# Performance work log

Hardware: AMD Instinct MI355X
Metric: run time of the kernel (lower is better)

Reference implementation:

```python
import jax, jax.numpy as jnp
import numpy as np

B, N, DIM = 2, 4096, 512
HEADS, DIM_HEAD = 8, 64
INNER = HEADS * DIM_HEAD  # 512
SCALE = DIM_HEAD ** -0.5
LN_EPS = 1e-5


def setup_inputs() -> dict:
    key = jax.random.key(0)
    ks = jax.random.split(key, 4)
    x = jax.random.normal(ks[0], (B, N, DIM), dtype=jnp.float32)
    # weights stored as [in, out] for plain matmul
    w_qkv = jax.random.normal(ks[1], (DIM, 3 * INNER), dtype=jnp.float32) * (DIM ** -0.5)
    ln_gamma = jnp.ones((INNER,), dtype=jnp.float32)
    ln_beta = jnp.zeros((INNER,), dtype=jnp.float32)
    w_out = jax.random.normal(ks[2], (INNER, DIM), dtype=jnp.float32) * (INNER ** -0.5)
    b_out = jnp.zeros((DIM,), dtype=jnp.float32)
    return {"x": x, "w_qkv": w_qkv, "ln_gamma": ln_gamma, "ln_beta": ln_beta,
            "w_out": w_out, "b_out": b_out}


def _layernorm(x, gamma, beta):
    mu = jnp.mean(x, axis=-1, keepdims=True)
    var = jnp.mean(jnp.square(x - mu), axis=-1, keepdims=True)
    return (x - mu) * jax.lax.rsqrt(var + LN_EPS) * gamma + beta


def reference(x, w_qkv, ln_gamma, ln_beta, w_out, b_out):
    b, n, _ = x.shape
    qkv = x @ w_qkv                                   # [b, n, 3*inner]
    q, k, v = jnp.split(qkv, 3, axis=-1)
    def to_heads(t):
        return t.reshape(b, n, HEADS, DIM_HEAD).transpose(0, 2, 1, 3)  # [b,h,n,d]
    q, k, v = to_heads(q), to_heads(k), to_heads(v)
    dots = jnp.einsum('bhid,bhjd->bhij', q, k) * SCALE  # [b,h,n,n]
    attn = jax.nn.relu(dots)                            # non-softmax rectified attention
    out = jnp.einsum('bhij,bhjd->bhid', attn, v)        # [b,h,n,d]
    out = out.transpose(0, 2, 1, 3).reshape(b, n, INNER)
    out = _layernorm(out, ln_gamma, ln_beta)
    return out @ w_out + b_out                          # [b,n,dim]
```

## Files before the change

kernel.cpp:

```cpp
#include <hip/hip_runtime.h>
#include <stdint.h>
#include <stddef.h>

typedef __bf16 bf16;
typedef bf16 bf16x4 __attribute__((ext_vector_type(4)));
typedef bf16 bf16x8 __attribute__((ext_vector_type(8)));
typedef float f32x4 __attribute__((ext_vector_type(4)));

#define DEVI static __device__ __forceinline__


DEVI f32x4 mfma16(bf16x8 a, bf16x8 b, f32x4 c) {
  return __builtin_amdgcn_mfma_f32_16x16x32_bf16(a, b, c, 0, 0, 0);
}

DEVI void gload_lds16(const bf16* g, bf16* lds) {
  __builtin_amdgcn_global_load_lds(
      (const __attribute__((address_space(1))) unsigned int*)g,
      (__attribute__((address_space(3))) unsigned int*)lds, 16, 0, 0);
}

DEVI int sigma64(int r) { return (r & 0x23) | ((r & 0xC) << 1) | ((r & 0x10) >> 2); }


__global__ __launch_bounds__(256) void cvt_kernel(const float* __restrict__ in,
                                                  bf16* __restrict__ out, int n4) {
  int i = blockIdx.x * blockDim.x + threadIdx.x;
  const int stride = gridDim.x * blockDim.x;
  for (; i < n4; i += stride) {
    f32x4 v = reinterpret_cast<const f32x4*>(in)[i];
    bf16x4 o;
    o[0] = (bf16)v[0]; o[1] = (bf16)v[1]; o[2] = (bf16)v[2]; o[3] = (bf16)v[3];
    reinterpret_cast<bf16x4*>(out)[i] = o;
  }
}

__global__ __launch_bounds__(256) void tcvt_kernel(const float* __restrict__ in,
                                                   bf16* __restrict__ out, int Kd, int Nd) {
  __shared__ bf16 T[64 * 80];
  const int k0 = blockIdx.y * 64, n0 = blockIdx.x * 64;
  const int r = threadIdx.x >> 2;
  const int c0 = (threadIdx.x & 3) * 16;
  const float* src = in + (size_t)(k0 + r) * Nd + n0 + c0;
#pragma unroll
  for (int j = 0; j < 16; ++j) T[(c0 + j) * 80 + r] = (bf16)src[j];
  __syncthreads();
  bf16* dst = out + (size_t)(n0 + r) * Kd + k0 + c0;
  const bf16* s = T + r * 80 + c0;
#pragma unroll
  for (int j = 0; j < 2; ++j)
    *reinterpret_cast<bf16x8*>(dst + j * 8) =
        *reinterpret_cast<const bf16x8*>(s + j * 8);
}

template <int EPI>
__global__ __launch_bounds__(256) void gemm_kernel(
    const bf16* __restrict__ A, const bf16* __restrict__ BT,
    bf16* __restrict__ qo, bf16* __restrict__ ko, bf16* __restrict__ vto,
    const float* __restrict__ bias, float* __restrict__ fo) {
  constexpr int K = 512;
  __shared__ __align__(16) bf16 SM[4 * 128 * 64];
  const int lane = threadIdx.x & 63;
  const int w = threadIdx.x >> 6;
  const int hi = lane >> 4;
  const int wm = w >> 1, wn = w & 1;
  const int m0 = blockIdx.y * 128, n0 = blockIdx.x * 128;
  const int sl = lane >> 3;
  const int ssc = ((lane & 7) ^ sl) * 8;

  auto AsB = [&](int bi) { return SM + bi * 8192; };
  auto BsB = [&](int bi) { return SM + 16384 + bi * 8192; };

  auto stage = [&](int bi, int kt) {
    const int k0 = kt * 64;
#pragma unroll
    for (int c = 0; c < 4; ++c) {
      const int ca = w * 4 + c;
      const int trow = ca * 8 + sl;
      gload_lds16(A + (size_t)(m0 + trow) * K + k0 + ssc, AsB(bi) + ca * 512);
      gload_lds16(BT + (size_t)(n0 + trow) * K + k0 + ssc, BsB(bi) + ca * 512);
    }
  };

  f32x4 acc[4][4];
#pragma unroll
  for (int i = 0; i < 4; ++i)
#pragma unroll
    for (int j = 0; j < 4; ++j) acc[i][j] = {0.f, 0.f, 0.f, 0.f};

  stage(0, 0);
  asm volatile("s_waitcnt vmcnt(0)" ::: "memory");
  __builtin_amdgcn_s_barrier();

  for (int kt = 0; kt < K / 64; ++kt) {
    const int cur = kt & 1;
    if (kt < K / 64 - 1) stage(cur ^ 1, kt + 1);
    const bf16* As = AsB(cur);
    const bf16* Bs = BsB(cur);
#pragma unroll
    for (int kc = 0; kc < 2; ++kc) {
      const int cs = kc * 4 + hi;
      const int csw = (cs ^ (lane & 7)) * 8;
      bf16x8 af[4], bfr[4];
#pragma unroll
      for (int mi = 0; mi < 4; ++mi)
        af[mi] = *reinterpret_cast<const bf16x8*>(
            &As[(wm * 64 + mi * 16 + (lane & 15)) * 64 + csw]);
#pragma unroll
      for (int ni = 0; ni < 4; ++ni)
        bfr[ni] = *reinterpret_cast<const bf16x8*>(
            &Bs[(wn * 64 + ni * 16 + (lane & 15)) * 64 + csw]);
      __builtin_amdgcn_s_setprio(1);
#pragma unroll
      for (int mi = 0; mi < 4; ++mi)
#pragma unroll
        for (int ni = 0; ni < 4; ++ni)
          acc[mi][ni] = mfma16(af[mi], bfr[ni], acc[mi][ni]);
      __builtin_amdgcn_s_setprio(0);
    }
    asm volatile("s_waitcnt vmcnt(0)" ::: "memory");
    __builtin_amdgcn_s_barrier();
  }

  if (EPI == 0) {
    if (n0 < 1024) {
#pragma unroll
      for (int mi = 0; mi < 4; ++mi)
#pragma unroll
        for (int ni = 0; ni < 4; ++ni)
#pragma unroll
          for (int r = 0; r < 4; ++r) {
            const int rl = wm * 64 + mi * 16 + hi * 4 + r;
            const int cl = wn * 64 + ni * 16 + (lane & 15);
            SM[rl * 136 + cl] = (bf16)acc[mi][ni][r];
          }
      __syncthreads();
      const int rl = threadIdx.x >> 1, hh = threadIdx.x & 1;
      const int m = m0 + rl, b = m >> 12, n = m & 4095;
      const int colg = n0 + hh * 64;
      const int sec = colg >> 9, h = (colg & 511) >> 6;
      bf16* dst = (sec ? ko : qo) + ((size_t)(b * 8 + h) * 4096 + n) * 64;
      const bf16* srcp = SM + rl * 136 + hh * 64;
#pragma unroll
      for (int j = 0; j < 8; ++j)
        *reinterpret_cast<bf16x8*>(dst + j * 8) =
            *reinterpret_cast<const bf16x8*>(srcp + j * 8);
    } else {
#pragma unroll
      for (int mi = 0; mi < 4; ++mi)
#pragma unroll
        for (int ni = 0; ni < 4; ++ni)
#pragma unroll
          for (int r = 0; r < 4; ++r) {
            const int rl = wm * 64 + mi * 16 + hi * 4 + r;
            const int cl = wn * 64 + ni * 16 + (lane & 15);
            SM[cl * 136 + rl] = (bf16)acc[mi][ni][r];
          }
      __syncthreads();
      const int b = m0 >> 12, nb = m0 & 4095;
      const int cl = threadIdx.x >> 1, half = threadIdx.x & 1;
      const int jj = (n0 - 1024) + cl, h = jj >> 6, d = jj & 63;
      bf16* dst = vto + ((size_t)(b * 8 + h) * 64 + d) * 4096 + nb + half * 64;
      const bf16* srcp = SM + cl * 136 + half * 64;
#pragma unroll
      for (int j = 0; j < 8; ++j)
        *reinterpret_cast<bf16x8*>(dst + j * 8) =
            *reinterpret_cast<const bf16x8*>(srcp + j * 8);
    }
    return;
  }

#pragma unroll
  for (int mi = 0; mi < 4; ++mi) {
#pragma unroll
    for (int ni = 0; ni < 4; ++ni) {
#pragma unroll
      for (int r = 0; r < 4; ++r) {
        const int m = m0 + wm * 64 + mi * 16 + hi * 4 + r;
        const int col = n0 + wn * 64 + ni * 16 + (lane & 15);
        fo[(size_t)m * 512 + col] = acc[mi][ni][r] + bias[col];
      }
    }
  }
}

__global__ __launch_bounds__(256, 4) void attn_kernel(
    const bf16* __restrict__ Q, const bf16* __restrict__ Kg,
    const bf16* __restrict__ VT, float* __restrict__ out0,
    float* __restrict__ out1) {
  __shared__ __align__(16) bf16 Ks[2 * 64 * 64];
  __shared__ __align__(16) bf16 Vs[2 * 64 * 64];
  const int lane = threadIdx.x & 63;
  const int w = threadIdx.x >> 6;
  const int hi = lane >> 4;
  const int ql = lane & 15;
  const int bh = blockIdx.y;
  const int q0 = blockIdx.x * 128 + w * 32;
  const int kvbase = blockIdx.z * 2048;
  const bf16* Qh = Q + (size_t)bh * 4096 * 64;
  const bf16* Kh = Kg + (size_t)bh * 4096 * 64;
  const bf16* Vh = VT + (size_t)bh * 64 * 4096;
  float* outp = blockIdx.z ? out1 : out0;

  const int sl = lane >> 3;
  const int ssc = ((lane & 7) ^ sl) * 8;

  int soff[4];
  if (w < 2) {
#pragma unroll
    for (int c = 0; c < 4; ++c) {
      const int rho = (w * 4 + c) * 8 + sl;
      soff[c] = sigma64(rho) * 64 + ssc;
    }
  } else {
#pragma unroll
    for (int c = 0; c < 4; ++c) {
      const int d = ((w - 2) * 4 + c) * 8 + sl;
      soff[c] = d * 4096 + ssc;
    }
  }

  auto stage = [&](int bi, int kv0) {
    if (w < 2) {
      bf16* KsB = Ks + bi * 4096;
#pragma unroll
      for (int c = 0; c < 4; ++c)
        gload_lds16(Kh + (size_t)kv0 * 64 + soff[c], KsB + (w * 4 + c) * 512);
    } else {
      bf16* VsB = Vs + bi * 4096;
#pragma unroll
      for (int c = 0; c < 4; ++c)
        gload_lds16(Vh + kv0 + soff[c], VsB + ((w - 2) * 4 + c) * 512);
    }
  };

  bf16x8 qf[2][2];
#pragma unroll
  for (int qb = 0; qb < 2; ++qb)
#pragma unroll
    for (int kc = 0; kc < 2; ++kc)
      qf[qb][kc] = *reinterpret_cast<const bf16x8*>(
          &Qh[(size_t)(q0 + qb * 16 + ql) * 64 + kc * 32 + hi * 8]);

  f32x4 o[2][4];
#pragma unroll
  for (int qb = 0; qb < 2; ++qb)
#pragma unroll
    for (int db = 0; db < 4; ++db) o[qb][db] = {0.f, 0.f, 0.f, 0.f};

  stage(0, kvbase);
  asm volatile("s_waitcnt vmcnt(0)" ::: "memory");
  __builtin_amdgcn_s_barrier();

  for (int it = 0; it < 32; ++it) {
    const int kv0 = kvbase + it * 64;
    const int cur = it & 1;
    const bf16* KsC = Ks + cur * 4096;
    const bf16* VsC = Vs + cur * 4096;
    if (it < 31) stage(cur ^ 1, kv0 + 64);

    f32x4 s[2][4];
#pragma unroll
    for (int qb = 0; qb < 2; ++qb)
#pragma unroll
      for (int kvb = 0; kvb < 4; ++kvb) s[qb][kvb] = {0.f, 0.f, 0.f, 0.f};
#pragma unroll
    for (int kc = 0; kc < 2; ++kc) {
      const int csw = ((kc * 4 + hi) ^ (lane & 7)) * 8;
      bf16x8 kf[4];
#pragma unroll
      for (int kvb = 0; kvb < 4; ++kvb)
        kf[kvb] = *reinterpret_cast<const bf16x8*>(
            &KsC[(kvb * 16 + ql) * 64 + csw]);
      __builtin_amdgcn_s_setprio(1);
#pragma unroll
      for (int qb = 0; qb < 2; ++qb)
#pragma unroll
        for (int kvb = 0; kvb < 4; ++kvb)
          s[qb][kvb] = mfma16(kf[kvb], qf[qb][kc], s[qb][kvb]);
      __builtin_amdgcn_s_setprio(0);
    }

#pragma unroll
    for (int kc = 0; kc < 2; ++kc) {
      const int csw = ((kc * 4 + hi) ^ (lane & 7)) * 8;
      bf16x8 vf[4];
#pragma unroll
      for (int db = 0; db < 4; ++db)
        vf[db] = *reinterpret_cast<const bf16x8*>(
            &VsC[(db * 16 + ql) * 64 + csw]);
      bf16x8 pa[2];
#pragma unroll
      for (int qb = 0; qb < 2; ++qb)
#pragma unroll
        for (int u = 0; u < 2; ++u)
#pragma unroll
          for (int r = 0; r < 4; ++r)
            pa[qb][u * 4 + r] = (bf16)fmaxf(s[qb][2 * kc + u][r], 0.f);
      __builtin_amdgcn_s_setprio(1);
#pragma unroll
      for (int qb = 0; qb < 2; ++qb)
#pragma unroll
        for (int db = 0; db < 4; ++db)
          o[qb][db] = mfma16(pa[qb], vf[db], o[qb][db]);
      __builtin_amdgcn_s_setprio(0);
    }

    asm volatile("s_waitcnt vmcnt(0)" ::: "memory");
    __builtin_amdgcn_s_barrier();
  }

  const int b = bh >> 3, h = bh & 7;
#pragma unroll
  for (int qb = 0; qb < 2; ++qb)
#pragma unroll
    for (int db = 0; db < 4; ++db)
#pragma unroll
      for (int r = 0; r < 4; ++r) {
        const int n = q0 + qb * 16 + hi * 4 + r;
        const int dcol = db * 16 + ql;
        outp[((size_t)(b * 4096 + n)) * 512 + h * 64 + dcol] = o[qb][db][r] * 0.125f;
      }
}

__global__ __launch_bounds__(256) void ln_kernel(const float* __restrict__ in0,
                                                 const float* __restrict__ in1,
                                                 const float* __restrict__ gamma,
                                                 const float* __restrict__ beta,
                                                 bf16* __restrict__ out) {
  const int lane = threadIdx.x & 63;
  const int w = threadIdx.x >> 6;
  const int row = blockIdx.x * 4 + w;
  const float* r0 = in0 + (size_t)row * 512;
  const float* r1 = in1 + (size_t)row * 512;
  f32x4 a = *reinterpret_cast<const f32x4*>(&r0[lane * 4]);
  f32x4 b = *reinterpret_cast<const f32x4*>(&r0[256 + lane * 4]);
  f32x4 a1 = *reinterpret_cast<const f32x4*>(&r1[lane * 4]);
  f32x4 b1 = *reinterpret_cast<const f32x4*>(&r1[256 + lane * 4]);
#pragma unroll
  for (int i = 0; i < 4; ++i) { a[i] += a1[i]; b[i] += b1[i]; }
  float s = a[0] + a[1] + a[2] + a[3] + b[0] + b[1] + b[2] + b[3];
  float ss = a[0] * a[0] + a[1] * a[1] + a[2] * a[2] + a[3] * a[3] +
             b[0] * b[0] + b[1] * b[1] + b[2] * b[2] + b[3] * b[3];
#pragma unroll
  for (int off = 32; off > 0; off >>= 1) {
    s += __shfl_xor(s, off);
    ss += __shfl_xor(ss, off);
  }
  const float mean = s * (1.f / 512.f);
  const float var = ss * (1.f / 512.f) - mean * mean;
  const float rstd = rsqrtf(var + 1e-5f);
  f32x4 g0 = *reinterpret_cast<const f32x4*>(&gamma[lane * 4]);
  f32x4 g1 = *reinterpret_cast<const f32x4*>(&gamma[256 + lane * 4]);
  f32x4 e0 = *reinterpret_cast<const f32x4*>(&beta[lane * 4]);
  f32x4 e1 = *reinterpret_cast<const f32x4*>(&beta[256 + lane * 4]);
  bf16x4 o0, o1;
#pragma unroll
  for (int i = 0; i < 4; ++i) {
    o0[i] = (bf16)((a[i] - mean) * rstd * g0[i] + e0[i]);
    o1[i] = (bf16)((b[i] - mean) * rstd * g1[i] + e1[i]);
  }
  *reinterpret_cast<bf16x4*>(&out[(size_t)row * 512 + lane * 4]) = o0;
  *reinterpret_cast<bf16x4*>(&out[(size_t)row * 512 + 256 + lane * 4]) = o1;
}

extern "C" void kernel_launch(void* const* d_in, const int* in_sizes, int n_in,
                              void* d_out, int out_size, void* d_ws, size_t ws_size,
                              hipStream_t stream) {
  const float* x = (const float*)d_in[0];
  const float* w_qkv = (const float*)d_in[1];
  const float* ln_g = (const float*)d_in[2];
  const float* ln_b = (const float*)d_in[3];
  const float* w_out = (const float*)d_in[4];
  const float* b_out = (const float*)d_in[5];
  float* out = (float*)d_out;

  char* ws = (char*)d_ws;
  size_t off = 0;
  auto alloc = [&](size_t bytes) {
    void* p = ws + off;
    off += (bytes + 255) & ~(size_t)255;
    return p;
  };
  bf16* x_bf = (bf16*)alloc((size_t)8192 * 512 * 2);
  bf16* wqkvT = (bf16*)alloc((size_t)1536 * 512 * 2);
  bf16* woutT = (bf16*)alloc((size_t)512 * 512 * 2);
  bf16* qbuf = (bf16*)alloc((size_t)16 * 4096 * 64 * 2);
  bf16* kbuf = (bf16*)alloc((size_t)16 * 4096 * 64 * 2);
  bf16* vtbuf = (bf16*)alloc((size_t)16 * 64 * 4096 * 2);
  float* attn_out0 = (float*)alloc((size_t)8192 * 512 * 4);
  float* attn_out1 = (float*)alloc((size_t)8192 * 512 * 4);
  bf16* ln_bf = (bf16*)alloc((size_t)8192 * 512 * 2);

  cvt_kernel<<<2048, 256, 0, stream>>>(x, x_bf, 8192 * 512 / 4);
  tcvt_kernel<<<dim3(24, 8), 256, 0, stream>>>(w_qkv, wqkvT, 512, 1536);
  tcvt_kernel<<<dim3(8, 8), 256, 0, stream>>>(w_out, woutT, 512, 512);

  gemm_kernel<0><<<dim3(12, 64), 256, 0, stream>>>(x_bf, wqkvT, qbuf, kbuf, vtbuf,
                                                   nullptr, nullptr);

  attn_kernel<<<dim3(32, 16, 2), 256, 0, stream>>>(qbuf, kbuf, vtbuf,
                                                   attn_out0, attn_out1);

  ln_kernel<<<2048, 256, 0, stream>>>(attn_out0, attn_out1, ln_g, ln_b, ln_bf);

  gemm_kernel<1><<<dim3(4, 64), 256, 0, stream>>>(ln_bf, woutT, nullptr, nullptr,
                                                  nullptr, b_out, out);
}
```

Before: 182.5 us.

## Prefetch two tiles ahead in GEMM and attention; merge prep conversion kernels

The GEMM and attention main loops now issue loads for both double-buffer slots up front. Each iteration waits with a partial vmcnt, so the next tile's loads stay in flight while the current tile is computed, and a slot is refilled right after the trailing barrier. The attention kernel also precomputes its global pointers and LDS read offsets to cut address arithmetic. The three fp32-to-bf16 conversion launches are merged into one prep kernel, which removes two launches. The vmcnt counts must match the number of loads issued per stage, or the loop reads stale LDS.

Result: no change. 180.4 us (-1.1%).

```diff
diff --git a/kernel.cpp b/kernel.cpp
--- a/kernel.cpp
+++ b/kernel.cpp
@@ -23,22 +23,9 @@
 DEVI int sigma64(int r) { return (r & 0x23) | ((r & 0xC) << 1) | ((r & 0x10) >> 2); }
 
 
-__global__ __launch_bounds__(256) void cvt_kernel(const float* __restrict__ in,
-                                                  bf16* __restrict__ out, int n4) {
-  int i = blockIdx.x * blockDim.x + threadIdx.x;
-  const int stride = gridDim.x * blockDim.x;
-  for (; i < n4; i += stride) {
-    f32x4 v = reinterpret_cast<const f32x4*>(in)[i];
-    bf16x4 o;
-    o[0] = (bf16)v[0]; o[1] = (bf16)v[1]; o[2] = (bf16)v[2]; o[3] = (bf16)v[3];
-    reinterpret_cast<bf16x4*>(out)[i] = o;
-  }
-}
-
-__global__ __launch_bounds__(256) void tcvt_kernel(const float* __restrict__ in,
-                                                   bf16* __restrict__ out, int Kd, int Nd) {
-  __shared__ bf16 T[64 * 80];
-  const int k0 = blockIdx.y * 64, n0 = blockIdx.x * 64;
+DEVI void tcvt_tile(const float* __restrict__ in, bf16* __restrict__ out,
+                    int Kd, int Nd, int bx, int by, bf16* T) {
+  const int k0 = by * 64, n0 = bx * 64;
   const int r = threadIdx.x >> 2;
   const int c0 = (threadIdx.x & 3) * 16;
   const float* src = in + (size_t)(k0 + r) * Nd + n0 + c0;
@@ -51,6 +38,30 @@
   for (int j = 0; j < 2; ++j)
     *reinterpret_cast<bf16x8*>(dst + j * 8) =
         *reinterpret_cast<const bf16x8*>(s + j * 8);
+}
+
+__global__ __launch_bounds__(256) void prep_kernel(
+    const float* __restrict__ x, bf16* __restrict__ xb,
+    const float* __restrict__ wq, bf16* __restrict__ wqT,
+    const float* __restrict__ wo, bf16* __restrict__ woT) {
+  __shared__ bf16 T[64 * 80];
+  const int blk = blockIdx.x;
+  if (blk < 2048) {
+    int i = blk * 256 + threadIdx.x;
+    const int n4 = 8192 * 512 / 4, stride = 2048 * 256;
+    for (; i < n4; i += stride) {
+      f32x4 v = reinterpret_cast<const f32x4*>(x)[i];
+      bf16x4 o;
+      o[0] = (bf16)v[0]; o[1] = (bf16)v[1]; o[2] = (bf16)v[2]; o[3] = (bf16)v[3];
+      reinterpret_cast<bf16x4*>(xb)[i] = o;
+    }
+  } else if (blk < 2240) {
+    const int t = blk - 2048;
+    tcvt_tile(wq, wqT, 512, 1536, t % 24, t / 24, T);
+  } else {
+    const int t = blk - 2240;
+    tcvt_tile(wo, woT, 512, 512, t % 8, t / 8, T);
+  }
 }
 
 template <int EPI>
@@ -89,18 +100,21 @@
     for (int j = 0; j < 4; ++j) acc[i][j] = {0.f, 0.f, 0.f, 0.f};
 
   stage(0, 0);
-  asm volatile("s_waitcnt vmcnt(0)" ::: "memory");
-  __builtin_amdgcn_s_barrier();
-
-  for (int kt = 0; kt < K / 64; ++kt) {
+  stage(1, 1);
+
+  for (int kt = 0; kt < 8; ++kt) {
     const int cur = kt & 1;
-    if (kt < K / 64 - 1) stage(cur ^ 1, kt + 1);
+    if (kt < 7) {
+      asm volatile("s_waitcnt vmcnt(8)" ::: "memory");
+    } else {
+      asm volatile("s_waitcnt vmcnt(0)" ::: "memory");
+    }
+    __builtin_amdgcn_s_barrier();
     const bf16* As = AsB(cur);
     const bf16* Bs = BsB(cur);
 #pragma unroll
     for (int kc = 0; kc < 2; ++kc) {
-      const int cs = kc * 4 + hi;
-      const int csw = (cs ^ (lane & 7)) * 8;
+      const int csw = ((kc * 4 + hi) ^ (lane & 7)) * 8;
       bf16x8 af[4], bfr[4];
 #pragma unroll
       for (int mi = 0; mi < 4; ++mi)
@@ -118,8 +132,8 @@
           acc[mi][ni] = mfma16(af[mi], bfr[ni], acc[mi][ni]);
       __builtin_amdgcn_s_setprio(0);
     }
-    asm volatile("s_waitcnt vmcnt(0)" ::: "memory");
     __builtin_amdgcn_s_barrier();
+    if (kt + 2 < 8) stage(cur, kt + 2);
   }
 
   if (EPI == 0) {
@@ -171,25 +185,22 @@
   }
 
 #pragma unroll
-  for (int mi = 0; mi < 4; ++mi) {
-#pragma unroll
-    for (int ni = 0; ni < 4; ++ni) {
+  for (int mi = 0; mi < 4; ++mi)
+#pragma unroll
+    for (int ni = 0; ni < 4; ++ni)
 #pragma unroll
       for (int r = 0; r < 4; ++r) {
         const int m = m0 + wm * 64 + mi * 16 + hi * 4 + r;
         const int col = n0 + wn * 64 + ni * 16 + (lane & 15);
         fo[(size_t)m * 512 + col] = acc[mi][ni][r] + bias[col];
       }
-    }
-  }
 }
 
 __global__ __launch_bounds__(256, 4) void attn_kernel(
     const bf16* __restrict__ Q, const bf16* __restrict__ Kg,
     const bf16* __restrict__ VT, float* __restrict__ out0,
     float* __restrict__ out1) {
-  __shared__ __align__(16) bf16 Ks[2 * 64 * 64];
-  __shared__ __align__(16) bf16 Vs[2 * 64 * 64];
+  __shared__ __align__(16) bf16 KV[4 * 4096];
   const int lane = threadIdx.x & 63;
   const int w = threadIdx.x >> 6;
   const int hi = lane >> 4;
@@ -205,34 +216,38 @@
   const int sl = lane >> 3;
   const int ssc = ((lane & 7) ^ sl) * 8;
 
-  int soff[4];
+  const bf16* gs[4];
+  int dstoff[4], step;
   if (w < 2) {
 #pragma unroll
     for (int c = 0; c < 4; ++c) {
       const int rho = (w * 4 + c) * 8 + sl;
-      soff[c] = sigma64(rho) * 64 + ssc;
-    }
+      gs[c] = Kh + (size_t)(kvbase + sigma64(rho)) * 64 + ssc;
+      dstoff[c] = (w * 4 + c) * 512;
+    }
+    step = 64 * 64;
   } else {
 #pragma unroll
     for (int c = 0; c < 4; ++c) {
       const int d = ((w - 2) * 4 + c) * 8 + sl;
-      soff[c] = d * 4096 + ssc;
-    }
-  }
-
-  auto stage = [&](int bi, int kv0) {
-    if (w < 2) {
-      bf16* KsB = Ks + bi * 4096;
-#pragma unroll
-      for (int c = 0; c < 4; ++c)
-        gload_lds16(Kh + (size_t)kv0 * 64 + soff[c], KsB + (w * 4 + c) * 512);
-    } else {
-      bf16* VsB = Vs + bi * 4096;
-#pragma unroll
-      for (int c = 0; c < 4; ++c)
-        gload_lds16(Vh + kv0 + soff[c], VsB + ((w - 2) * 4 + c) * 512);
+      gs[c] = Vh + (size_t)d * 4096 + kvbase + ssc;
+      dstoff[c] = 8192 + ((w - 2) * 4 + c) * 512;
+    }
+    step = 64;
+  }
+
+  auto stageN = [&](int bi) {
+#pragma unroll
+    for (int c = 0; c < 4; ++c) {
+      gload_lds16(gs[c], KV + bi * 4096 + dstoff[c]);
+      gs[c] += step;
     }
   };
+
+  int lro[2];
+#pragma unroll
+  for (int kc = 0; kc < 2; ++kc)
+    lro[kc] = ql * 64 + (((kc * 4 + hi) ^ (lane & 7)) * 8);
 
   bf16x8 qf[2][2];
 #pragma unroll
@@ -248,16 +263,19 @@
 #pragma unroll
     for (int db = 0; db < 4; ++db) o[qb][db] = {0.f, 0.f, 0.f, 0.f};
 
-  stage(0, kvbase);
-  asm volatile("s_waitcnt vmcnt(0)" ::: "memory");
-  __builtin_amdgcn_s_barrier();
+  stageN(0);
+  stageN(1);
 
   for (int it = 0; it < 32; ++it) {
-    const int kv0 = kvbase + it * 64;
     const int cur = it & 1;
-    const bf16* KsC = Ks + cur * 4096;
-    const bf16* VsC = Vs + cur * 4096;
-    if (it < 31) stage(cur ^ 1, kv0 + 64);
+    if (it < 31) {
+      asm volatile("s_waitcnt vmcnt(4)" ::: "memory");
+    } else {
+      asm volatile("s_waitcnt vmcnt(0)" ::: "memory");
+    }
+    __builtin_amdgcn_s_barrier();
+
+    const bf16* Kb = KV + cur * 4096;
 
     f32x4 s[2][4];
 #pragma unroll
@@ -266,12 +284,11 @@
       for (int kvb = 0; kvb < 4; ++kvb) s[qb][kvb] = {0.f, 0.f, 0.f, 0.f};
 #pragma unroll
     for (int kc = 0; kc < 2; ++kc) {
-      const int csw = ((kc * 4 + hi) ^ (lane & 7)) * 8;
+      const bf16* kbp = Kb + lro[kc];
       bf16x8 kf[4];
 #pragma unroll
       for (int kvb = 0; kvb < 4; ++kvb)
-        kf[kvb] = *reinterpret_cast<const bf16x8*>(
-            &KsC[(kvb * 16 + ql) * 64 + csw]);
+        kf[kvb] = *reinterpret_cast<const bf16x8*>(kbp + kvb * 1024);
       __builtin_amdgcn_s_setprio(1);
 #pragma unroll
       for (int qb = 0; qb < 2; ++qb)
@@ -283,12 +300,11 @@
 
 #pragma unroll
     for (int kc = 0; kc < 2; ++kc) {
-      const int csw = ((kc * 4 + hi) ^ (lane & 7)) * 8;
+      const bf16* vbp = Kb + 8192 + lro[kc];
       bf16x8 vf[4];
 #pragma unroll
       for (int db = 0; db < 4; ++db)
-        vf[db] = *reinterpret_cast<const bf16x8*>(
-            &VsC[(db * 16 + ql) * 64 + csw]);
+        vf[db] = *reinterpret_cast<const bf16x8*>(vbp + db * 1024);
       bf16x8 pa[2];
 #pragma unroll
       for (int qb = 0; qb < 2; ++qb)
@@ -306,8 +322,8 @@
       __builtin_amdgcn_s_setprio(0);
     }
 
-    asm volatile("s_waitcnt vmcnt(0)" ::: "memory");
     __builtin_amdgcn_s_barrier();
+    if (it + 2 < 32) stageN(cur);
   }
 
   const int b = bh >> 3, h = bh & 7;
@@ -392,9 +408,7 @@
   float* attn_out1 = (float*)alloc((size_t)8192 * 512 * 4);
   bf16* ln_bf = (bf16*)alloc((size_t)8192 * 512 * 2);
 
-  cvt_kernel<<<2048, 256, 0, stream>>>(x, x_bf, 8192 * 512 / 4);
-  tcvt_kernel<<<dim3(24, 8), 256, 0, stream>>>(w_qkv, wqkvT, 512, 1536);
-  tcvt_kernel<<<dim3(8, 8), 256, 0, stream>>>(w_out, woutT, 512, 512);
+  prep_kernel<<<2304, 256, 0, stream>>>(x, x_bf, w_qkv, wqkvT, w_out, woutT);
 
   gemm_kernel<0><<<dim3(12, 64), 256, 0, stream>>>(x_bf, wqkvT, qbuf, kbuf, vtbuf,
                                                    nullptr, nullptr);
```
